# Optimization experiments

Hardware: AMD Instinct MI355X
Metric: run time of the kernel (lower is better)

Reference implementation:

```python
import jax, jax.numpy as jnp
import numpy as np

B, S, E, H = 2, 2048, 1024, 16
DH = E // H  # 64


def setup_inputs() -> dict:
    key = jax.random.key(0)
    ks = jax.random.split(key, 5)
    scale = 1.0 / np.sqrt(E)
    x = jax.random.normal(ks[0], (B, S, E), dtype=jnp.float32)
    # stacked per-head kqv Linear weights: out = x @ Wkqv[h] + bkqv[h], producing (k, q, v) chunks
    Wkqv = jax.random.normal(ks[1], (H, E, 3 * DH), dtype=jnp.float32) * scale
    bkqv = jax.random.normal(ks[2], (H, 3 * DH), dtype=jnp.float32) * scale
    Wo = jax.random.normal(ks[3], (E, E), dtype=jnp.float32) * scale
    bo = jax.random.normal(ks[4], (E,), dtype=jnp.float32) * scale
    return {"x": x, "Wkqv": Wkqv, "bkqv": bkqv, "Wo": Wo, "bo": bo}


def reference(x, Wkqv, bkqv, Wo, bo):
    b, s, e = x.shape
    h, _, f = Wkqv.shape
    dh = f // 3
    # per-head projection, fused over heads: [b, h, s, 3*dh]
    kqv = jnp.einsum('bse,hef->bhsf', x, Wkqv) + bkqv[None, :, None, :]
    # chunk order in the original is k, q, v
    k, q, v = jnp.split(kqv, 3, axis=-1)
    scores = jnp.einsum('bhqd,bhkd->bhqk', q, k) / jnp.sqrt(jnp.asarray(dh, x.dtype))
    causal = jnp.tril(jnp.ones((s, s), dtype=bool))  # slice of the tril buffer
    scores = jnp.where(causal[None, None], scores, -jnp.inf)
    weights = jax.nn.softmax(scores, axis=-1)
    sa = jnp.einsum('bhqk,bhkd->bhqd', weights, v)
    # concat heads along feature dim (head order preserved)
    sa = sa.transpose(0, 2, 1, 3).reshape(b, s, h * dh)
    return sa @ Wo + bo
```

## Files before the change

kernel.cpp:

```cpp
#include <hip/hip_runtime.h>
#include <hip/hip_bf16.h>

typedef __attribute__((ext_vector_type(8))) short bf16x8;
typedef __attribute__((ext_vector_type(4))) float f32x4;
typedef __attribute__((ext_vector_type(2))) unsigned u32x2;
typedef __attribute__((ext_vector_type(4))) unsigned u32x4;
typedef unsigned short u16;

#define NEG_INF (-__builtin_inff())

__device__ __forceinline__ void gload16(const void* g, void* l) {
  __builtin_amdgcn_global_load_lds(
      (const __attribute__((address_space(1))) void*)g,
      (__attribute__((address_space(3))) void*)l, 16, 0, 0);
}

__device__ __forceinline__ u16 f2b(float f) {
  union { float f; unsigned u; } v;
  v.f = f;
  unsigned r = v.u + 0x7fff + ((v.u >> 16) & 1);
  return (u16)(r >> 16);
}

__device__ __forceinline__ unsigned cvt_pk_bf16(float a, float b) {
  unsigned r;
  asm("v_cvt_pk_bf16_f32 %0, %1, %2" : "=v"(r) : "v"(a), "v"(b));
  return r;
}

__global__ __launch_bounds__(256) void prep_kernel(
    const float* __restrict__ x, u16* __restrict__ xb,
    const float* __restrict__ Wkqv, u16* __restrict__ WkqvT,
    const float* __restrict__ Wo, u16* __restrict__ WoT) {
  __shared__ u16 t[32][33];
  const int bid = blockIdx.x;
  const int tid = threadIdx.x;
  if (bid < 4096) {
    const int i = bid * 256 + tid;
    float4 v = ((const float4*)x)[i];
    ushort2 a = {f2b(v.x), f2b(v.y)}, b = {f2b(v.z), f2b(v.w)};
    ((ushort2*)xb)[i * 2] = a;
    ((ushort2*)xb)[i * 2 + 1] = b;
    return;
  }
  const int tx = tid & 31, ty = tid >> 5;
  const float* src;
  u16* dst;
  int R, C, bx_, by;
  if (bid < 7168) {
    const int tt = bid - 4096;
    const int bz = tt / 192, rem = tt % 192;
    by = rem / 6; bx_ = rem % 6; R = 1024; C = 192;
    src = Wkqv + (size_t)bz * R * C;
    dst = WkqvT + (size_t)bz * R * C;
  } else {
    const int tt = bid - 7168;
    by = tt >> 5; bx_ = tt & 31; R = 1024; C = 1024;
    src = Wo; dst = WoT;
  }
  const int c0 = bx_ * 32, r0 = by * 32;
  for (int i = ty; i < 32; i += 8)
    t[i][tx] = f2b(src[(size_t)(r0 + i) * C + c0 + tx]);
  __syncthreads();
  for (int i = ty; i < 32; i += 8)
    dst[(size_t)(c0 + i) * R + r0 + tx] = t[tx][i];
}

__device__ __forceinline__ void gemm_mainloop_128(
    const __hip_bfloat16* __restrict__ A, const __hip_bfloat16* __restrict__ Bt,
    int K, int m0, int n0, f32x4 acc[4][4], char* AsB, char* BsB) {
  const int tid = threadIdx.x;
  const int wave = tid >> 6, lane = tid & 63;
  const int lhi = lane >> 4, llo = lane & 15;
  const int wr = wave >> 1, wc = wave & 1;
  f32x4 z = {0.f, 0.f, 0.f, 0.f};
#pragma unroll
  for (int i = 0; i < 4; i++)
#pragma unroll
    for (int j = 0; j < 4; j++) acc[i][j] = z;

#define GSTAGE(c, kk)                                                          \
  {                                                                            \
    char* AsW = AsB + (c)*8192;                                                \
    char* BsW = BsB + (c)*8192;                                                \
    _Pragma("unroll") for (int i = 0; i < 2; i++) {                            \
      int cb = i * 256 + wave * 64;                                            \
      int cq = cb + lane;                                                      \
      gload16(A + ((size_t)(m0 + (cq >> 2)) * K + (kk) + (cq & 3) * 8),        \
              AsW + cb * 16);                                                  \
      gload16(Bt + ((size_t)(n0 + (cq >> 2)) * K + (kk) + (cq & 3) * 8),       \
              BsW + cb * 16);                                                  \
    }                                                                          \
  }

  GSTAGE(0, 0);
  int cur = 0;
  const int nk = K >> 5;
  for (int t = 0; t < nk; t++) {
    if (t + 1 < nk) {
      GSTAGE(cur ^ 1, (t + 1) * 32);
      asm volatile("s_waitcnt vmcnt(4)" ::: "memory");
    } else {
      asm volatile("s_waitcnt vmcnt(0)" ::: "memory");
    }
    __builtin_amdgcn_s_barrier();
    __builtin_amdgcn_sched_barrier(0);

    const char* Ar = AsB + cur * 8192;
    const char* Br = BsB + cur * 8192;
    bf16x8 a[4], b[4];
#pragma unroll
    for (int m4 = 0; m4 < 4; m4++)
      a[m4] = *(const bf16x8*)(Ar + (wr * 64 + m4 * 16 + llo) * 64 + lhi * 16);
#pragma unroll
    for (int n4 = 0; n4 < 4; n4++)
      b[n4] = *(const bf16x8*)(Br + (wc * 64 + n4 * 16 + llo) * 64 + lhi * 16);
#pragma unroll
    for (int m4 = 0; m4 < 4; m4++)
#pragma unroll
      for (int n4 = 0; n4 < 4; n4++)
        acc[m4][n4] =
            __builtin_amdgcn_mfma_f32_16x16x32_bf16(a[m4], b[n4], acc[m4][n4], 0, 0, 0);
    __builtin_amdgcn_sched_barrier(0);
    __builtin_amdgcn_s_barrier();
    cur ^= 1;
  }
#undef GSTAGE
}

__device__ __forceinline__ void gemm_mainloop_64x128(
    const __hip_bfloat16* __restrict__ A, const __hip_bfloat16* __restrict__ Bt,
    int K, int m0, int n0, f32x4 acc[2][4], char* AsB, char* BsB) {
  const int tid = threadIdx.x;
  const int wave = tid >> 6, lane = tid & 63;
  const int lhi = lane >> 4, llo = lane & 15;
  const int wr = wave >> 1, wc = wave & 1;
  f32x4 z = {0.f, 0.f, 0.f, 0.f};
#pragma unroll
  for (int i = 0; i < 2; i++)
#pragma unroll
    for (int j = 0; j < 4; j++) acc[i][j] = z;

#define GSTAGE64(c, kk)                                                        \
  {                                                                            \
    char* AsW = AsB + (c)*4096;                                                \
    char* BsW = BsB + (c)*8192;                                                \
    gload16(A + ((size_t)(m0 + (tid >> 2)) * K + (kk) + (tid & 3) * 8),        \
            AsW + (wave * 64) * 16);                                           \
    _Pragma("unroll") for (int i = 0; i < 2; i++) {                            \
      int cb = i * 256 + wave * 64;                                            \
      int cq = cb + lane;                                                      \
      gload16(Bt + ((size_t)(n0 + (cq >> 2)) * K + (kk) + (cq & 3) * 8),       \
              BsW + cb * 16);                                                  \
    }                                                                          \
  }

  GSTAGE64(0, 0);
  int cur = 0;
  const int nk = K >> 5;
  for (int t = 0; t < nk; t++) {
    if (t + 1 < nk) {
      GSTAGE64(cur ^ 1, (t + 1) * 32);
      asm volatile("s_waitcnt vmcnt(3)" ::: "memory");
    } else {
      asm volatile("s_waitcnt vmcnt(0)" ::: "memory");
    }
    __builtin_amdgcn_s_barrier();
    __builtin_amdgcn_sched_barrier(0);

    const char* Ar = AsB + cur * 4096;
    const char* Br = BsB + cur * 8192;
    bf16x8 a[2], b[4];
#pragma unroll
    for (int m2 = 0; m2 < 2; m2++)
      a[m2] = *(const bf16x8*)(Ar + (wr * 32 + m2 * 16 + llo) * 64 + lhi * 16);
#pragma unroll
    for (int n4 = 0; n4 < 4; n4++)
      b[n4] = *(const bf16x8*)(Br + (wc * 64 + n4 * 16 + llo) * 64 + lhi * 16);
#pragma unroll
    for (int m2 = 0; m2 < 2; m2++)
#pragma unroll
      for (int n4 = 0; n4 < 4; n4++)
        acc[m2][n4] =
            __builtin_amdgcn_mfma_f32_16x16x32_bf16(a[m2], b[n4], acc[m2][n4], 0, 0, 0);
    __builtin_amdgcn_sched_barrier(0);
    __builtin_amdgcn_s_barrier();
    cur ^= 1;
  }
#undef GSTAGE64
}

__global__ __launch_bounds__(256) void kqv_gemm(
    const __hip_bfloat16* __restrict__ x, const __hip_bfloat16* __restrict__ WT,
    const float* __restrict__ bkqv, __hip_bfloat16* __restrict__ Qb,
    __hip_bfloat16* __restrict__ Kb, __hip_bfloat16* __restrict__ Vt) {
  __shared__ __align__(16) char ldsbuf[34816];
  const int m0 = blockIdx.y * 128, n0 = blockIdx.x * 128;
  f32x4 acc[4][4];
  gemm_mainloop_128(x, WT, 1024, m0, n0, acc, ldsbuf, ldsbuf + 16384);

  const int tid = threadIdx.x, wave = tid >> 6, lane = tid & 63;
  const int lhi = lane >> 4, llo = lane & 15;
  const int wr = wave >> 1, wc = wave & 1;
  u16* Vsw = (u16*)ldsbuf;
#pragma unroll
  for (int m4 = 0; m4 < 4; m4++)
#pragma unroll
    for (int n4 = 0; n4 < 4; n4++)
#pragma unroll
      for (int r = 0; r < 4; r++) {
        int sp = wr * 64 + m4 * 16 + lhi * 4 + r;
        int row = wc * 64 + n4 * 16 + llo;
        int mg = m0 + sp;
        int ng = n0 + row;
        int b = mg >> 11, s = mg & 2047;
        int h = ng / 192, f = ng % 192;
        float v = acc[m4][n4][r] + bkqv[h * 192 + f];
        int d = f & 63;
        size_t bh = (size_t)(b * 16 + h);
        if (f < 64)
          Kb[(bh * 2048 + s) * 64 + d] = __float2bfloat16(v);
        else if (f < 128)
          Qb[(bh * 2048 + s) * 64 + d] = __float2bfloat16(v * 0.180336880f);
        else
          Vsw[row * 136 + sp] = f2b(v);
      }
  __syncthreads();
#pragma unroll
  for (int it = 0; it < 8; it++) {
    int task = it * 256 + tid;
    int row = task >> 4, c = task & 15;
    int ng = n0 + row, f = ng % 192;
    if (f >= 128) {
      int h = ng / 192, d = f - 128;
      int mg0 = m0 + c * 8;
      int b = mg0 >> 11, s = mg0 & 2047;
      size_t bh = (size_t)(b * 16 + h);
      u32x4 w = *(const u32x4*)&Vsw[row * 136 + c * 8];
      *(u32x4*)((u16*)Vt + (size_t)(bh * 64 + d) * 2048 + s) = w;
    }
  }
}

__global__ __launch_bounds__(256) void attn_kernel(
    const __hip_bfloat16* __restrict__ Qb, const __hip_bfloat16* __restrict__ Kb,
    const __hip_bfloat16* __restrict__ Vt, __hip_bfloat16* __restrict__ SA) {
  __shared__ __align__(16) char lds[32768];
  const int orig = blockIdx.x;
  const int bh = (orig & 7) * 4 + ((orig >> 3) & 3);
  const int qt = 31 - (orig >> 5);
  const int nt = qt + 1;
  const int b = bh >> 4, h = bh & 15;
  const int tid = threadIdx.x, wave = tid >> 6, lane = tid & 63;
  const int lhi = lane >> 4, llo = lane & 15;
  const int lhi4 = lhi * 4;

  const __hip_bfloat16* qp =
      Qb + ((size_t)bh * 2048 + qt * 64 + wave * 16 + llo) * 64 + lhi * 8;
  bf16x8 q0 = *(const bf16x8*)qp, q1 = *(const bf16x8*)(qp + 32);

  const char* Kg = (const char*)(Kb + (size_t)bh * 2048 * 64);
  const char* Vg = (const char*)(Vt + (size_t)bh * 64 * 2048);

  f32x4 z = {0.f, 0.f, 0.f, 0.f};
  f32x4 o[4];
  float m_s = NEG_INF, l_s = 0.f;
#pragma unroll
  for (int i = 0; i < 4; i++) o[i] = z;
  const int qg = qt * 64 + wave * 16 + llo;
  const int qg0 = qt * 64 + wave * 16 + lhi4;

#define STAGE(c, k0)                                                          \
  {                                                                           \
    char* KsW = lds + (c)*8192;                                               \
    char* VsW = lds + 16384 + (c)*8192;                                       \
    _Pragma("unroll") for (int i = 0; i < 2; i++) {                           \
      int ch = i * 256 + tid;                                                 \
      int soff = (ch * 16) ^ (((ch >> 3) & 7) << 4);                          \
      gload16(Kg + (size_t)(k0)*128 + soff, KsW + (i * 256 + wave * 64) * 16);\
      int dd = ch >> 3, c8 = ch & 7;                                          \
      int boff = (c8 * 16) ^ ((dd & 7) << 4);                                 \
      gload16(Vg + (size_t)dd * 4096 + (size_t)(k0)*2 + boff,                 \
              VsW + (i * 256 + wave * 64) * 16);                              \
    }                                                                         \
  }

  STAGE(0, 0);
  int cur = 0;

  for (int T = 0; T < nt; T++) {
    if (T + 1 < nt) {
      STAGE(cur ^ 1, (T + 1) * 64);
      asm volatile("s_waitcnt vmcnt(4)" ::: "memory");
    } else {
      asm volatile("s_waitcnt vmcnt(0)" ::: "memory");
    }
    __builtin_amdgcn_s_barrier();
    __builtin_amdgcn_sched_barrier(0);

    const int k0 = T * 64;
    const bool masked = (T == nt - 1);
    const char* KsB = lds + cur * 8192;
    const char* VsB = lds + 16384 + cur * 8192;

    f32x4 s[4] = {z, z, z, z};
#pragma unroll
    for (int j = 0; j < 4; j++) {
      const int row = j * 16 + llo;
      const int rx = (row & 7) << 4;
      bf16x8 bk0 = *(const bf16x8*)(KsB + ((row * 128 + lhi * 16) ^ rx));
      bf16x8 bk1 = *(const bf16x8*)(KsB + ((row * 128 + 64 + lhi * 16) ^ rx));
      s[j] = __builtin_amdgcn_mfma_f32_16x16x32_bf16(bk0, q0, s[j], 0, 0, 0);
      s[j] = __builtin_amdgcn_mfma_f32_16x16x32_bf16(bk1, q1, s[j], 0, 0, 0);
    }

    if (masked) {
#pragma unroll
      for (int j = 0; j < 4; j++)
#pragma unroll
        for (int r = 0; r < 4; r++)
          if (k0 + j * 16 + lhi4 + r > qg) s[j][r] = NEG_INF;
    }
    float pmax = s[0][0];
#pragma unroll
    for (int j = 0; j < 4; j++)
#pragma unroll
      for (int r = 0; r < 4; r++) pmax = fmaxf(pmax, s[j][r]);
    {
      union { float f; unsigned u; } pu;
      pu.f = pmax;
      u32x2 sp = __builtin_amdgcn_permlane32_swap(pu.u, pu.u, false, false);
      float m1 = fmaxf(__uint_as_float(sp.x), __uint_as_float(sp.y));
      union { float f; unsigned u; } mu;
      mu.f = m1;
      u32x2 tp = __builtin_amdgcn_permlane16_swap(mu.u, mu.u, false, false);
      pmax = fmaxf(__uint_as_float(tp.x), __uint_as_float(tp.y));
    }
    if (!__all(pmax - m_s <= 5.0f)) {
      const float mn = fmaxf(m_s, pmax);
      const float sc = __builtin_exp2f(m_s - mn);
      m_s = mn;
      l_s *= sc;
#pragma unroll
      for (int r = 0; r < 4; r++) {
        const float scr = __shfl(sc, lhi4 + r);
#pragma unroll
        for (int n4 = 0; n4 < 4; n4++) o[n4][r] *= scr;
      }
    }

    unsigned pk[4][2];
    float ps = 0.f;
#pragma unroll
    for (int j = 0; j < 4; j++) {
      float p0 = __builtin_exp2f(s[j][0] - m_s);
      float p1 = __builtin_exp2f(s[j][1] - m_s);
      float p2 = __builtin_exp2f(s[j][2] - m_s);
      float p3 = __builtin_exp2f(s[j][3] - m_s);
      ps += (p0 + p1) + (p2 + p3);
      pk[j][0] = cvt_pk_bf16(p0, p1);
      pk[j][1] = cvt_pk_bf16(p2, p3);
    }
    l_s += ps;

    u32x4 a0w, a1w;
#pragma unroll
    for (int u = 0; u < 2; u++) {
      u32x2 sp = __builtin_amdgcn_permlane32_swap(pk[0][u], pk[1][u], false, false);
      u32x2 tp = __builtin_amdgcn_permlane16_swap(sp.x, sp.y, false, false);
      a0w[u] = tp.x;
      a0w[u + 2] = tp.y;
    }
#pragma unroll
    for (int u = 0; u < 2; u++) {
      u32x2 sp = __builtin_amdgcn_permlane32_swap(pk[2][u], pk[3][u], false, false);
      u32x2 tp = __builtin_amdgcn_permlane16_swap(sp.x, sp.y, false, false);
      a1w[u] = tp.x;
      a1w[u + 2] = tp.y;
    }
    bf16x8 ap0 = __builtin_bit_cast(bf16x8, a0w);
    bf16x8 ap1 = __builtin_bit_cast(bf16x8, a1w);

#pragma unroll
    for (int n4 = 0; n4 < 4; n4++) {
      const int d = n4 * 16 + llo;
      const int dx = (d & 7) << 4;
      bf16x8 bv0 = *(const bf16x8*)(VsB + ((d * 128 + lhi * 16) ^ dx));
      bf16x8 bv1 = *(const bf16x8*)(VsB + ((d * 128 + 64 + lhi * 16) ^ dx));
      o[n4] = __builtin_amdgcn_mfma_f32_16x16x32_bf16(ap0, bv0, o[n4], 0, 0, 0);
      o[n4] = __builtin_amdgcn_mfma_f32_16x16x32_bf16(ap1, bv1, o[n4], 0, 0, 0);
    }
    __builtin_amdgcn_sched_barrier(0);
    __builtin_amdgcn_s_barrier();
    cur ^= 1;
  }

  {
    union { float f; unsigned u; } lu;
    lu.f = l_s;
    u32x2 sp = __builtin_amdgcn_permlane32_swap(lu.u, lu.u, false, false);
    float l1 = __uint_as_float(sp.x) + __uint_as_float(sp.y);
    union { float f; unsigned u; } l2u;
    l2u.f = l1;
    u32x2 tp = __builtin_amdgcn_permlane16_swap(l2u.u, l2u.u, false, false);
    const float l = __uint_as_float(tp.x) + __uint_as_float(tp.y);
    const float inv = 1.f / l;
#pragma unroll
    for (int r = 0; r < 4; r++) {
      const float invr = __shfl(inv, lhi4 + r);
      const size_t ob = ((size_t)b * 2048 + qg0 + r) * 1024 + h * 64;
#pragma unroll
      for (int n4 = 0; n4 < 4; n4++)
        SA[ob + n4 * 16 + llo] = __float2bfloat16(o[n4][r] * invr);
    }
  }
#undef STAGE
}

__global__ __launch_bounds__(256) void out_gemm(
    const __hip_bfloat16* __restrict__ SA, const __hip_bfloat16* __restrict__ WoT,
    const float* __restrict__ bo, float* __restrict__ out) {
  __shared__ __align__(16) char As[8192];
  __shared__ __align__(16) char Bs[16384];
  const int m0 = blockIdx.y * 64, n0 = blockIdx.x * 128;
  f32x4 acc[2][4];
  gemm_mainloop_64x128(SA, WoT, 1024, m0, n0, acc, As, Bs);

  const int tid = threadIdx.x, wave = tid >> 6, lane = tid & 63;
  const int lhi = lane >> 4, llo = lane & 15;
  const int wr = wave >> 1, wc = wave & 1;
#pragma unroll
  for (int m2 = 0; m2 < 2; m2++)
#pragma unroll
    for (int n4 = 0; n4 < 4; n4++)
#pragma unroll
      for (int r = 0; r < 4; r++) {
        int mg = m0 + wr * 32 + m2 * 16 + lhi * 4 + r;
        int ng = n0 + wc * 64 + n4 * 16 + llo;
        out[(size_t)mg * 1024 + ng] = acc[m2][n4][r] + bo[ng];
      }
}

extern "C" void kernel_launch(void* const* d_in, const int* in_sizes, int n_in,
                              void* d_out, int out_size, void* d_ws, size_t ws_size,
                              hipStream_t stream) {
  const float* x = (const float*)d_in[0];
  const float* Wkqv = (const float*)d_in[1];
  const float* bkqv = (const float*)d_in[2];
  const float* Wo = (const float*)d_in[3];
  const float* bo = (const float*)d_in[4];
  float* out = (float*)d_out;

  char* w = (char*)d_ws;
  __hip_bfloat16* WkqvT = (__hip_bfloat16*)(w);
  __hip_bfloat16* WoT = (__hip_bfloat16*)(w + 6291456);
  __hip_bfloat16* Qb = (__hip_bfloat16*)(w + 8388608);
  __hip_bfloat16* Kb = (__hip_bfloat16*)(w + 16777216);
  __hip_bfloat16* Vt = (__hip_bfloat16*)(w + 25165824);
  __hip_bfloat16* SAb = (__hip_bfloat16*)(w + 33554432);
  __hip_bfloat16* xb = (__hip_bfloat16*)(w + 41943040);

  prep_kernel<<<8192, 256, 0, stream>>>(x, (u16*)xb, Wkqv, (u16*)WkqvT,
                                        Wo, (u16*)WoT);
  kqv_gemm<<<dim3(24, 32), 256, 0, stream>>>(xb, WkqvT, bkqv, Qb, Kb, Vt);
  attn_kernel<<<1024, 256, 0, stream>>>(Qb, Kb, Vt, SAb);
  out_gemm<<<dim3(8, 64), 256, 0, stream>>>(SAb, WoT, bo, out);
}
```

Measured before the change: 117.4 us.

## Software-pipeline attention: compute next tile's QK^T while softmaxing current tile

Restructures the attention main loop so the QK^T MFMAs for tile T+1 are issued before the softmax and PV of tile T, overlapping matrix-core work with the exp/max VALU work. K loads are staged two tiles ahead and V one tile ahead, using separate staging macros and adjusted vmcnt waits. This raises register pressure, since two score sets stay live at once, and makes the wait/barrier logic more delicate.

```diff
diff --git a/kernel.cpp b/kernel.cpp
--- a/kernel.cpp
+++ b/kernel.cpp
@@ -242,6 +242,76 @@
   }
 }
 
+__device__ __forceinline__ void softmax_pack(
+    f32x4* s, bool masked, int k0, int qg, int lhi4,
+    float& m_s, float& l_s, f32x4* o, bf16x8& ap0, bf16x8& ap1) {
+  if (masked) {
+#pragma unroll
+    for (int jj = 0; jj < 4; jj++)
+#pragma unroll
+      for (int r = 0; r < 4; r++)
+        if (k0 + jj * 16 + lhi4 + r > qg) s[jj][r] = NEG_INF;
+  }
+  float pmax = s[0][0];
+#pragma unroll
+  for (int jj = 0; jj < 4; jj++)
+#pragma unroll
+    for (int r = 0; r < 4; r++) pmax = fmaxf(pmax, s[jj][r]);
+  {
+    union { float f; unsigned u; } pu;
+    pu.f = pmax;
+    u32x2 sp = __builtin_amdgcn_permlane32_swap(pu.u, pu.u, false, false);
+    float m1 = fmaxf(__uint_as_float(sp.x), __uint_as_float(sp.y));
+    union { float f; unsigned u; } mu;
+    mu.f = m1;
+    u32x2 tp = __builtin_amdgcn_permlane16_swap(mu.u, mu.u, false, false);
+    pmax = fmaxf(__uint_as_float(tp.x), __uint_as_float(tp.y));
+  }
+  if (!__all(pmax - m_s <= 5.0f)) {
+    const float mn = fmaxf(m_s, pmax);
+    const float sc = __builtin_exp2f(m_s - mn);
+    m_s = mn;
+    l_s *= sc;
+#pragma unroll
+    for (int r = 0; r < 4; r++) {
+      const float scr = __shfl(sc, lhi4 + r);
+#pragma unroll
+      for (int n4 = 0; n4 < 4; n4++) o[n4][r] *= scr;
+    }
+  }
+  unsigned pk[4][2];
+  float ps = 0.f;
+#pragma unroll
+  for (int jj = 0; jj < 4; jj++) {
+    float p0 = __builtin_exp2f(s[jj][0] - m_s);
+    float p1 = __builtin_exp2f(s[jj][1] - m_s);
+    float p2 = __builtin_exp2f(s[jj][2] - m_s);
+    float p3 = __builtin_exp2f(s[jj][3] - m_s);
+    ps += (p0 + p1) + (p2 + p3);
+    pk[jj][0] = cvt_pk_bf16(p0, p1);
+    pk[jj][1] = cvt_pk_bf16(p2, p3);
+  }
+  l_s += ps;
+
+  u32x4 a0w, a1w;
+#pragma unroll
+  for (int u = 0; u < 2; u++) {
+    u32x2 sp = __builtin_amdgcn_permlane32_swap(pk[0][u], pk[1][u], false, false);
+    u32x2 tp = __builtin_amdgcn_permlane16_swap(sp.x, sp.y, false, false);
+    a0w[u] = tp.x;
+    a0w[u + 2] = tp.y;
+  }
+#pragma unroll
+  for (int u = 0; u < 2; u++) {
+    u32x2 sp = __builtin_amdgcn_permlane32_swap(pk[2][u], pk[3][u], false, false);
+    u32x2 tp = __builtin_amdgcn_permlane16_swap(sp.x, sp.y, false, false);
+    a1w[u] = tp.x;
+    a1w[u + 2] = tp.y;
+  }
+  ap0 = __builtin_bit_cast(bf16x8, a0w);
+  ap1 = __builtin_bit_cast(bf16x8, a1w);
+}
+
 __global__ __launch_bounds__(256) void attn_kernel(
     const __hip_bfloat16* __restrict__ Qb, const __hip_bfloat16* __restrict__ Kb,
     const __hip_bfloat16* __restrict__ Vt, __hip_bfloat16* __restrict__ SA) {
@@ -270,28 +340,64 @@
   const int qg = qt * 64 + wave * 16 + llo;
   const int qg0 = qt * 64 + wave * 16 + lhi4;
 
-#define STAGE(c, k0)                                                          \
+#define STAGE_K(c, k0)                                                        \
   {                                                                           \
-    char* KsW = lds + (c)*8192;                                               \
-    char* VsW = lds + 16384 + (c)*8192;                                       \
+    char* W = lds + (c)*8192;                                                 \
     _Pragma("unroll") for (int i = 0; i < 2; i++) {                           \
       int ch = i * 256 + tid;                                                 \
       int soff = (ch * 16) ^ (((ch >> 3) & 7) << 4);                          \
-      gload16(Kg + (size_t)(k0)*128 + soff, KsW + (i * 256 + wave * 64) * 16);\
+      gload16(Kg + (size_t)(k0)*128 + soff, W + (i * 256 + wave * 64) * 16);  \
+    }                                                                         \
+  }
+#define STAGE_V(c, k0)                                                        \
+  {                                                                           \
+    char* W = lds + 16384 + (c)*8192;                                         \
+    _Pragma("unroll") for (int i = 0; i < 2; i++) {                           \
+      int ch = i * 256 + tid;                                                 \
       int dd = ch >> 3, c8 = ch & 7;                                          \
       int boff = (c8 * 16) ^ ((dd & 7) << 4);                                 \
       gload16(Vg + (size_t)dd * 4096 + (size_t)(k0)*2 + boff,                 \
-              VsW + (i * 256 + wave * 64) * 16);                              \
+              W + (i * 256 + wave * 64) * 16);                                \
     }                                                                         \
   }
 
-  STAGE(0, 0);
-  int cur = 0;
+#define QKT(sdst, kc, setz)                                                   \
+  {                                                                           \
+    const char* KsB = lds + (kc)*8192;                                        \
+    _Pragma("unroll") for (int j = 0; j < 4; j++) {                           \
+      const int row = j * 16 + llo;                                           \
+      const int rx = (row & 7) << 4;                                          \
+      bf16x8 bk0 = *(const bf16x8*)(KsB + ((row * 128 + lhi * 16) ^ rx));     \
+      bf16x8 bk1 = *(const bf16x8*)(KsB + ((row * 128 + 64 + lhi * 16) ^ rx));\
+      if (setz) sdst[j] = z;                                                  \
+      sdst[j] = __builtin_amdgcn_mfma_f32_16x16x32_bf16(bk0, q0, sdst[j], 0, 0, 0); \
+      sdst[j] = __builtin_amdgcn_mfma_f32_16x16x32_bf16(bk1, q1, sdst[j], 0, 0, 0); \
+    }                                                                         \
+  }
+
+  f32x4 sprev[4];
+  STAGE_K(0, 0);
+  STAGE_V(0, 0);
+  if (nt > 1) {
+    STAGE_K(1, 64);
+    asm volatile("s_waitcnt vmcnt(4)" ::: "memory");
+  } else {
+    asm volatile("s_waitcnt vmcnt(2)" ::: "memory");
+  }
+  __builtin_amdgcn_s_barrier();
+  __builtin_amdgcn_sched_barrier(0);
+  QKT(sprev, 0, 1);
+  __builtin_amdgcn_sched_barrier(0);
+  __builtin_amdgcn_s_barrier();
 
   for (int T = 0; T < nt; T++) {
-    if (T + 1 < nt) {
-      STAGE(cur ^ 1, (T + 1) * 64);
+    if (T + 2 < nt) {
+      STAGE_K(T & 1, (T + 2) * 64);
+      STAGE_V((T + 1) & 1, (T + 1) * 64);
       asm volatile("s_waitcnt vmcnt(4)" ::: "memory");
+    } else if (T + 1 < nt) {
+      STAGE_V((T + 1) & 1, (T + 1) * 64);
+      asm volatile("s_waitcnt vmcnt(2)" ::: "memory");
     } else {
       asm volatile("s_waitcnt vmcnt(0)" ::: "memory");
     }
@@ -300,99 +406,31 @@
 
     const int k0 = T * 64;
     const bool masked = (T == nt - 1);
-    const char* KsB = lds + cur * 8192;
-    const char* VsB = lds + 16384 + cur * 8192;
-
-    f32x4 s[4] = {z, z, z, z};
-#pragma unroll
-    for (int j = 0; j < 4; j++) {
-      const int row = j * 16 + llo;
-      const int rx = (row & 7) << 4;
-      bf16x8 bk0 = *(const bf16x8*)(KsB + ((row * 128 + lhi * 16) ^ rx));
-      bf16x8 bk1 = *(const bf16x8*)(KsB + ((row * 128 + 64 + lhi * 16) ^ rx));
-      s[j] = __builtin_amdgcn_mfma_f32_16x16x32_bf16(bk0, q0, s[j], 0, 0, 0);
-      s[j] = __builtin_amdgcn_mfma_f32_16x16x32_bf16(bk1, q1, s[j], 0, 0, 0);
-    }
-
-    if (masked) {
-#pragma unroll
-      for (int j = 0; j < 4; j++)
-#pragma unroll
-        for (int r = 0; r < 4; r++)
-          if (k0 + j * 16 + lhi4 + r > qg) s[j][r] = NEG_INF;
-    }
-    float pmax = s[0][0];
-#pragma unroll
-    for (int j = 0; j < 4; j++)
-#pragma unroll
-      for (int r = 0; r < 4; r++) pmax = fmaxf(pmax, s[j][r]);
+
+    f32x4 snew[4];
+    if (T + 1 < nt) QKT(snew, (T + 1) & 1, 1);
+
+    bf16x8 ap0, ap1;
+    softmax_pack(sprev, masked, k0, qg, lhi4, m_s, l_s, o, ap0, ap1);
+
     {
-      union { float f; unsigned u; } pu;
-      pu.f = pmax;
-      u32x2 sp = __builtin_amdgcn_permlane32_swap(pu.u, pu.u, false, false);
-      float m1 = fmaxf(__uint_as_float(sp.x), __uint_as_float(sp.y));
-      union { float f; unsigned u; } mu;
-      mu.f = m1;
-      u32x2 tp = __builtin_amdgcn_permlane16_swap(mu.u, mu.u, false, false);
-      pmax = fmaxf(__uint_as_float(tp.x), __uint_as_float(tp.y));
-    }
-    if (!__all(pmax - m_s <= 5.0f)) {
-      const float mn = fmaxf(m_s, pmax);
-      const float sc = __builtin_exp2f(m_s - mn);
-      m_s = mn;
-      l_s *= sc;
-#pragma unroll
-      for (int r = 0; r < 4; r++) {
-        const float scr = __shfl(sc, lhi4 + r);
-#pragma unroll
-        for (int n4 = 0; n4 < 4; n4++) o[n4][r] *= scr;
+      const char* VsB = lds + 16384 + (T & 1) * 8192;
+#pragma unroll
+      for (int n4 = 0; n4 < 4; n4++) {
+        const int d = n4 * 16 + llo;
+        const int dx = (d & 7) << 4;
+        bf16x8 bv0 = *(const bf16x8*)(VsB + ((d * 128 + lhi * 16) ^ dx));
+        bf16x8 bv1 = *(const bf16x8*)(VsB + ((d * 128 + 64 + lhi * 16) ^ dx));
+        o[n4] = __builtin_amdgcn_mfma_f32_16x16x32_bf16(ap0, bv0, o[n4], 0, 0, 0);
+        o[n4] = __builtin_amdgcn_mfma_f32_16x16x32_bf16(ap1, bv1, o[n4], 0, 0, 0);
       }
     }
-
-    unsigned pk[4][2];
-    float ps = 0.f;
-#pragma unroll
-    for (int j = 0; j < 4; j++) {
-      float p0 = __builtin_exp2f(s[j][0] - m_s);
-      float p1 = __builtin_exp2f(s[j][1] - m_s);
-      float p2 = __builtin_exp2f(s[j][2] - m_s);
-      float p3 = __builtin_exp2f(s[j][3] - m_s);
-      ps += (p0 + p1) + (p2 + p3);
-      pk[j][0] = cvt_pk_bf16(p0, p1);
-      pk[j][1] = cvt_pk_bf16(p2, p3);
-    }
-    l_s += ps;
-
-    u32x4 a0w, a1w;
-#pragma unroll
-    for (int u = 0; u < 2; u++) {
-      u32x2 sp = __builtin_amdgcn_permlane32_swap(pk[0][u], pk[1][u], false, false);
-      u32x2 tp = __builtin_amdgcn_permlane16_swap(sp.x, sp.y, false, false);
-      a0w[u] = tp.x;
-      a0w[u + 2] = tp.y;
-    }
-#pragma unroll
-    for (int u = 0; u < 2; u++) {
-      u32x2 sp = __builtin_amdgcn_permlane32_swap(pk[2][u], pk[3][u], false, false);
-      u32x2 tp = __builtin_amdgcn_permlane16_swap(sp.x, sp.y, false, false);
-      a1w[u] = tp.x;
-      a1w[u + 2] = tp.y;
-    }
-    bf16x8 ap0 = __builtin_bit_cast(bf16x8, a0w);
-    bf16x8 ap1 = __builtin_bit_cast(bf16x8, a1w);
-
-#pragma unroll
-    for (int n4 = 0; n4 < 4; n4++) {
-      const int d = n4 * 16 + llo;
-      const int dx = (d & 7) << 4;
-      bf16x8 bv0 = *(const bf16x8*)(VsB + ((d * 128 + lhi * 16) ^ dx));
-      bf16x8 bv1 = *(const bf16x8*)(VsB + ((d * 128 + 64 + lhi * 16) ^ dx));
-      o[n4] = __builtin_amdgcn_mfma_f32_16x16x32_bf16(ap0, bv0, o[n4], 0, 0, 0);
-      o[n4] = __builtin_amdgcn_mfma_f32_16x16x32_bf16(ap1, bv1, o[n4], 0, 0, 0);
+    if (T + 1 < nt) {
+#pragma unroll
+      for (int j = 0; j < 4; j++) sprev[j] = snew[j];
     }
     __builtin_amdgcn_sched_barrier(0);
     __builtin_amdgcn_s_barrier();
-    cur ^= 1;
   }
 
   {
@@ -414,7 +452,9 @@
         SA[ob + n4 * 16 + llo] = __float2bfloat16(o[n4][r] * invr);
     }
   }
-#undef STAGE
+#undef STAGE_K
+#undef STAGE_V
+#undef QKT
 }
 
 __global__ __launch_bounds__(256) void out_gemm(
```

Result: no change. 119.6 us (+1.9%).
